# Optimization experiments

Hardware: AMD Instinct MI355X
Metric: run time of the kernel (lower is better)

## Reference

```python
import jax, jax.numpy as jnp
import numpy as np

N = 100_000      # nodes
E = 1_600_000    # edges
F_IN = 4         # num_features
H = 128          # hidden_channels
C = 5            # num_classes
G = 256          # graphs in batch


def setup_inputs() -> dict:
    key = jax.random.key(0)
    ks = jax.random.split(key, 14)
    x = jax.random.normal(ks[0], (N, F_IN), dtype=jnp.float32)
    edge_index = jax.random.randint(ks[1], (2, E), 0, N, dtype=jnp.int64)
    batch = jnp.sort(jax.random.randint(ks[2], (N,), 0, G, dtype=jnp.int64))
    def lin(k, fan_in, fan_out):
        kw, kb = jax.random.split(k)
        s = 1.0 / np.sqrt(fan_in)
        W = jax.random.uniform(kw, (fan_in, fan_out), jnp.float32, -s, s)
        b = jax.random.uniform(kb, (fan_out,), jnp.float32, -s, s)
        return W, b
    W1, b1 = lin(ks[3], F_IN, H)
    W2, b2 = lin(ks[4], H, H)
    W3, b3 = lin(ks[5], H, H)
    W4, b4 = lin(ks[6], H, H)
    Wl, bl = lin(ks[7], H, C)
    return {"x": x, "edge_index": edge_index, "batch": batch,
            "W1": W1, "b1": b1, "W2": W2, "b2": b2,
            "W3": W3, "b3": b3, "W4": W4, "b4": b4,
            "Wl": Wl, "bl": bl}


def reference(x, edge_index, batch, W1, b1, W2, b2, W3, b3, W4, b4, Wl, bl):
    n = x.shape[0]
    loop = jnp.arange(n, dtype=edge_index.dtype)
    src = jnp.concatenate([edge_index[0], loop])  # [E+N], with self-loops
    dst = jnp.concatenate([edge_index[1], loop])
    # symmetric normalization on A + I (PyG GCNConv default)
    deg = jax.ops.segment_sum(jnp.ones_like(dst, dtype=x.dtype), dst, num_segments=n)
    dinv = deg ** -0.5  # deg >= 1 thanks to self-loops
    coef = dinv[src] * dinv[dst]  # per-edge norm [E+N]

    def conv(h, W, b):
        h = h @ W                               # [N, H]
        msg = h[src] * coef[:, None]            # gather + scale [E+N, H]
        return jax.ops.segment_sum(msg, dst, num_segments=n) + b

    h = jax.nn.relu(conv(x, W1, b1))
    h = jax.nn.relu(conv(h, W2, b2))
    h = jax.nn.relu(conv(h, W3, b3))
    h = jax.nn.relu(conv(h, W4, b4))

    # global_mean_pool over graph ids
    counts = jax.ops.segment_sum(jnp.ones((n,), h.dtype), batch, num_segments=G)
    pooled = jax.ops.segment_sum(h, batch, num_segments=G)
    pooled = pooled / jnp.maximum(counts, 1.0)[:, None]  # [G, H]

    return jax.nn.sigmoid(pooled @ Wl + bl)  # [G, C]
```

## Files before the change

kernel.cpp:

```cpp
#include <hip/hip_runtime.h>
#include <hip/hip_fp8.h>
#include <math.h>

#define N_NODES 100000
#define N_EDGES 1600000
#define F_IN    4
#define HID     128
#define N_CLS   5
#define N_GRAPH 256
#define POOL_SEG 8

#define BSHIFT   9
#define BSIZE    512
#define NBUK     196
#define NCHUNK   200
#define CHUNK    8000

typedef _Float16 f16;
typedef _Float16 f16x2 __attribute__((ext_vector_type(2)));
typedef _Float16 f16x8 __attribute__((ext_vector_type(8)));
typedef float f32x4 __attribute__((ext_vector_type(4)));

__device__ __forceinline__ float rec_coef(unsigned r) {
    return (float)__builtin_bit_cast(_Float16, (unsigned short)(r & 0x7FFFu));
}

__device__ __forceinline__ f16x2 rec_coef2(unsigned r) {
    unsigned c = r & 0x7FFFu;
    return __builtin_bit_cast(f16x2, (c << 16) | c);
}

__device__ __forceinline__ float2 fp8x2_to_f32x2(unsigned short raw) {
    __hip_fp8x2_e4m3 t;
    t.__x = raw;
    return static_cast<float2>(t);
}

#if __has_builtin(__builtin_amdgcn_cvt_pk_f16_fp8)
__device__ __forceinline__ f16x2 cvt_h2(unsigned v) {
    auto t = __builtin_amdgcn_cvt_pk_f16_fp8((short)v);
    return __builtin_bit_cast(f16x2, t);
}
#else
__device__ __forceinline__ f16x2 cvt_h2(unsigned v) {
    float2 f = fp8x2_to_f32x2((unsigned short)v);
    auto t = __builtin_amdgcn_cvt_pkrtz(f.x, f.y);
    return __builtin_bit_cast(f16x2, t);
}
#endif

__device__ __forceinline__ void fma8h(f16x2 c2, uint2 v, f16x2* acc) {
    acc[0] += c2 * cvt_h2(v.x);
    acc[1] += c2 * cvt_h2(v.x >> 16);
    acc[2] += c2 * cvt_h2(v.y);
    acc[3] += c2 * cvt_h2(v.y >> 16);
}

__device__ __forceinline__ f16x2 shfl_xor_h2(f16x2 a, int m) {
    return __builtin_bit_cast(f16x2, __shfl_xor(__builtin_bit_cast(int, a), m, 64));
}

__global__ __launch_bounds__(256) void k_bc(const int* __restrict__ dst, int* __restrict__ C) {
    __shared__ int cnt[NBUK];
    int t = threadIdx.x;
    if (t < NBUK) cnt[t] = 0;
    __syncthreads();
    int base = blockIdx.x * CHUNK;
#pragma unroll
    for (int it = 0; it < 32; ++it) {
        int idx = it * 256 + t;
        if (idx < CHUNK) atomicAdd(&cnt[dst[base + idx] >> BSHIFT], 1);
    }
    __syncthreads();
    if (t < NBUK) C[blockIdx.x * NBUK + t] = cnt[t];
}

__global__ __launch_bounds__(256) void k_bscan(const int* __restrict__ C, int* __restrict__ Off,
                                               int* __restrict__ bbase) {
    __shared__ int s[256];
    int b = threadIdx.x;
    int tot = 0;
    if (b < NBUK) {
        for (int c = 0; c < NCHUNK; ++c) {
            Off[c * NBUK + b] = tot;
            tot += C[c * NBUK + b];
        }
    }
    s[b] = (b < NBUK) ? tot : 0;
    __syncthreads();
    for (int off = 1; off < 256; off <<= 1) {
        int v = (b >= off) ? s[b - off] : 0;
        __syncthreads();
        s[b] += v;
        __syncthreads();
    }
    if (b < NBUK) bbase[b] = s[b] - tot;
    if (b == 0) bbase[NBUK] = N_EDGES;
}

__global__ __launch_bounds__(256) void k_scatter(const int* __restrict__ src, const int* __restrict__ dst,
                                                 const int* __restrict__ Off, const int* __restrict__ bbase,
                                                 unsigned* __restrict__ bkt) {
    __shared__ int cur[NBUK];
    int t = threadIdx.x;
    if (t < NBUK) cur[t] = bbase[t] + Off[blockIdx.x * NBUK + t];
    __syncthreads();
    int base = blockIdx.x * CHUNK;
#pragma unroll
    for (int it = 0; it < 32; ++it) {
        int idx = it * 256 + t;
        if (idx < CHUNK) {
            int s = src[base + idx], d = dst[base + idx];
            int b = d >> BSHIFT;
            int p = atomicAdd(&cur[b], 1);
            bkt[p] = ((unsigned)s << BSHIFT) | (unsigned)(d & (BSIZE - 1));
        }
    }
}

__global__ __launch_bounds__(256) void k_hist2(const unsigned* __restrict__ bkt,
                                               const int* __restrict__ bbase,
                                               int* __restrict__ deg, float* __restrict__ dinv,
                                               int* __restrict__ padTot) {
    __shared__ int hist[BSIZE];
    __shared__ int tot;
    int t = threadIdx.x, b = blockIdx.x;
    hist[t] = 0; hist[t + 256] = 0;
    if (t == 0) tot = 0;
    __syncthreads();
    int s0 = bbase[b], s1 = bbase[b + 1];
    for (int e = s0 + t; e < s1; e += 256) atomicAdd(&hist[bkt[e] & (BSIZE - 1)], 1);
    __syncthreads();
    int loc = 0;
#pragma unroll
    for (int h = 0; h < 2; ++h) {
        int l = t + h * 256;
        int node = b * BSIZE + l;
        int d = hist[l];
        if (node < N_NODES) {
            deg[node] = d;
            dinv[node] = rsqrtf((float)d + 1.0f);
        }
        loc += (d + 7) >> 3;
    }
    atomicAdd(&tot, loc);
    __syncthreads();
    if (t == 0) padTot[b] = tot << 3;
}

__global__ __launch_bounds__(256) void k_pscan(const int* __restrict__ padTot, int* __restrict__ padBase,
                                               int* __restrict__ rowptrP) {
    __shared__ int s[256];
    int b = threadIdx.x;
    int v = (b < NBUK) ? padTot[b] : 0;
    s[b] = v;
    __syncthreads();
    for (int off = 1; off < 256; off <<= 1) {
        int u = (b >= off) ? s[b - off] : 0;
        __syncthreads();
        s[b] += u;
        __syncthreads();
    }
    if (b < NBUK) padBase[b] = s[b] - v;
    if (b == 0) {
        padBase[NBUK] = s[NBUK - 1];
        rowptrP[N_NODES] = s[NBUK - 1];
    }
}

__global__ __launch_bounds__(256) void k_local2(const unsigned* __restrict__ bkt,
                                                const int* __restrict__ bbase,
                                                const int* __restrict__ deg,
                                                const float* __restrict__ dinv,
                                                const int* __restrict__ padBase,
                                                int* __restrict__ rowptrP,
                                                unsigned* __restrict__ edges) {
    __shared__ int sc[BSIZE];
    __shared__ int cur[BSIZE];
    __shared__ int st[BSIZE];
    __shared__ float dv[BSIZE];
    int t = threadIdx.x, b = blockIdx.x;
    int base = padBase[b];
    int n0 = b * BSIZE + t, n1 = n0 + 256;
    int d0 = (n0 < N_NODES) ? deg[n0] : 0;
    int d1 = (n1 < N_NODES) ? deg[n1] : 0;
    int p0 = ((d0 + 7) >> 3) << 3;
    int p1 = ((d1 + 7) >> 3) << 3;
    sc[t] = p0; sc[t + 256] = p1;
    dv[t] = (n0 < N_NODES) ? dinv[n0] : 0.f;
    dv[t + 256] = (n1 < N_NODES) ? dinv[n1] : 0.f;
    __syncthreads();
    for (int off = 1; off < BSIZE; off <<= 1) {
        int i0 = t, i1 = t + 256;
        int v0 = (i0 >= off) ? sc[i0 - off] : 0;
        int v1 = (i1 >= off) ? sc[i1 - off] : 0;
        __syncthreads();
        sc[i0] += v0; sc[i1] += v1;
        __syncthreads();
    }
    int off0 = base + sc[t] - p0;
    int off1 = base + sc[t + 256] - p1;
    if (n0 < N_NODES) rowptrP[n0] = off0;
    if (n1 < N_NODES) rowptrP[n1] = off1;
    cur[t] = off0; cur[t + 256] = off1;
    st[t]  = off0; st[t + 256]  = off1;
    int padT = sc[BSIZE - 1];
    for (int i = base + t; i < base + padT; i += 256) edges[i] = 0;
    __syncthreads();
    int s0 = bbase[b], s1 = bbase[b + 1];
    for (int e = s0 + t; e < s1; e += 256) {
        unsigned r = bkt[e];
        int dl = (int)(r & (BSIZE - 1));
        int s = (int)(r >> BSHIFT);
        int p = atomicAdd(&cur[dl], 1);
        int rs = st[dl];
        int sl = p - rs;
        int phys = rs + (sl & ~7) + (((sl & 1) << 2) | ((sl >> 1) & 3));
        float c = dv[dl] * dinv[s];
        unsigned short cb = __builtin_bit_cast(unsigned short, (f16)c);
        edges[phys] = ((unsigned)s << 15) | (unsigned)(cb & 0x7FFFu);
    }
}

__global__ __launch_bounds__(256) void k_aggx1(const float4* __restrict__ x,
                                               const int* __restrict__ rowptrP,
                                               const unsigned* __restrict__ edges,
                                               const float* __restrict__ dinv,
                                               const float* __restrict__ W1, const float* __restrict__ b1,
                                               unsigned* __restrict__ hA) {
    __shared__ float4 sxa[16];
    __shared__ float sW[4 * HID];
    __shared__ float sb[HID];
    int t = threadIdx.x;
    sW[t] = W1[t];
    sW[t + 256] = W1[t + 256];
    if (t < HID) sb[t] = b1[t];
    int grp = t >> 4;
    int l = t & 15;
    int node = blockIdx.x * 16 + grp;
    int beg = rowptrP[node], end = rowptrP[node + 1];
    float ax = 0.f, ay = 0.f, az = 0.f, aw = 0.f;
    for (int e = beg + l; e < end; e += 16) {
        unsigned r = edges[e];
        float c = rec_coef(r);
        float4 v = x[r >> 15];
        ax = fmaf(c, v.x, ax); ay = fmaf(c, v.y, ay);
        az = fmaf(c, v.z, az); aw = fmaf(c, v.w, aw);
    }
#pragma unroll
    for (int off = 1; off < 16; off <<= 1) {
        ax += __shfl_xor(ax, off, 64);
        ay += __shfl_xor(ay, off, 64);
        az += __shfl_xor(az, off, 64);
        aw += __shfl_xor(aw, off, 64);
    }
    if (l == 0) {
        float di = dinv[node];
        float c0 = di * di;
        float4 xv = x[node];
        sxa[grp] = make_float4(fmaf(c0, xv.x, ax), fmaf(c0, xv.y, ay),
                               fmaf(c0, xv.z, az), fmaf(c0, xv.w, aw));
    }
    __syncthreads();

    int node0 = blockIdx.x * 16;
#pragma unroll
    for (int it = 0; it < 2; ++it) {
        int id = it * 256 + t;
        int n = id >> 5;
        int g = id & 31;
        float4 a = sxa[n];
        float c[4];
#pragma unroll
        for (int j = 0; j < 4; ++j) {
            int col = g * 4 + j;
            float v = sb[col];
            v = fmaf(a.x, sW[col],           v);
            v = fmaf(a.y, sW[HID + col],     v);
            v = fmaf(a.z, sW[2 * HID + col], v);
            v = fmaf(a.w, sW[3 * HID + col], v);
            c[j] = fmaxf(v, 0.0f);
        }
        unsigned lo = __hip_fp8x2_e4m3(make_float2(c[0], c[1])).__x;
        unsigned hi = __hip_fp8x2_e4m3(make_float2(c[2], c[3])).__x;
        hA[(node0 + n) * 32 + g] = lo | (hi << 16);
    }
}

template <bool FP8OUT>
__global__ __launch_bounds__(512, 8) void k_aggemm8(const unsigned* __restrict__ h8,
                                                    const int* __restrict__ rowptrP,
                                                    const unsigned* __restrict__ edges,
                                                    const float* __restrict__ dinv,
                                                    const f16* __restrict__ Wp,
                                                    const float* __restrict__ bias,
                                                    void* __restrict__ outv) {
    __shared__ f16 S[16 * HID];
    int wave = threadIdx.x >> 6;
    int lane = threadIdx.x & 63;
    int half = lane >> 5;
    int g    = (lane >> 4) & 1;
    int l    = lane & 15;
    int node0 = blockIdx.x * 16;
    int row   = wave * 2 + half;
    int node  = node0 + row;
    int beg = rowptrP[node];
    int end = rowptrP[node + 1];
    const char* hp = (const char*)h8 + l * 8;

    f16x2 acc[4];
    acc[0] = (f16x2){0, 0}; acc[1] = (f16x2){0, 0};
    acc[2] = (f16x2){0, 0}; acc[3] = (f16x2){0, 0};
    {
        float di = dinv[node];
        f16 c0 = (g == 0) ? (f16)(di * di) : (f16)0.f;
        f16x2 c02; c02.x = c0; c02.y = c0;
        uint2 v = *(const uint2*)(hp + ((size_t)node << 7));
        fma8h(c02, v, acc);
    }

    if (beg < end) {
        uint4 R = *(const uint4*)(edges + beg + g * 4);
        uint2 V0 = *(const uint2*)(hp + ((R.x >> 8) & 0xFFFFFF80u));
        uint2 V1 = *(const uint2*)(hp + ((R.y >> 8) & 0xFFFFFF80u));
        uint2 V2 = *(const uint2*)(hp + ((R.z >> 8) & 0xFFFFFF80u));
        uint2 V3 = *(const uint2*)(hp + ((R.w >> 8) & 0xFFFFFF80u));
        int e = beg;
        while (true) {
            int en = e + 8;
            bool more = en < end;
            uint4 Rc = R;
            uint2 W0 = V0, W1 = V1, W2 = V2, W3 = V3;
            if (more) R = *(const uint4*)(edges + en + g * 4);
            fma8h(rec_coef2(Rc.x), W0, acc);
            fma8h(rec_coef2(Rc.y), W1, acc);
            fma8h(rec_coef2(Rc.z), W2, acc);
            fma8h(rec_coef2(Rc.w), W3, acc);
            if (!more) break;
            V0 = *(const uint2*)(hp + ((R.x >> 8) & 0xFFFFFF80u));
            V1 = *(const uint2*)(hp + ((R.y >> 8) & 0xFFFFFF80u));
            V2 = *(const uint2*)(hp + ((R.z >> 8) & 0xFFFFFF80u));
            V3 = *(const uint2*)(hp + ((R.w >> 8) & 0xFFFFFF80u));
            e = en;
        }
    }

#pragma unroll
    for (int j = 0; j < 4; ++j) acc[j] += shfl_xor_h2(acc[j], 16);

    if ((lane & 16) == 0) {
        f16x8 o;
        o[0] = acc[0][0]; o[1] = acc[0][1]; o[2] = acc[1][0]; o[3] = acc[1][1];
        o[4] = acc[2][0]; o[5] = acc[2][1]; o[6] = acc[3][0]; o[7] = acc[3][1];
        int dw = (l * 4) ^ ((row & 7) << 2);
        *(f16x8*)&S[row * HID + dw * 2] = o;
    }
    __syncthreads();

    {
        int t = wave;
        int m = lane & 15;
        int q = lane >> 4;
        f32x4 c4 = (f32x4){0.f, 0.f, 0.f, 0.f};
#pragma unroll
        for (int ks = 0; ks < 4; ++ks) {
            int dw = (ks * 16 + q * 4) ^ ((m & 7) << 2);
            f16x8 a = *(const f16x8*)&S[m * HID + dw * 2];
            f16x8 b = *(const f16x8*)(Wp + ((size_t)(t * 4 + ks) * 64 + lane) * 8);
            c4 = __builtin_amdgcn_mfma_f32_16x16x32_f16(a, b, c4, 0, 0, 0);
        }
        float bb = bias[t * 16 + m];
#pragma unroll
        for (int r = 0; r < 4; ++r) {
            float val = fmaxf(c4[r] + bb, 0.0f);
            int orow = node0 + q * 4 + r;
            if constexpr (FP8OUT) {
                ((__hip_fp8_e4m3*)outv)[(size_t)orow * HID + t * 16 + m] = __hip_fp8_e4m3(val);
            } else {
                ((f16*)outv)[(size_t)orow * HID + t * 16 + m] = (f16)val;
            }
        }
    }
}

__global__ __launch_bounds__(256) void k_packW3(const float* __restrict__ W2, const float* __restrict__ W3,
                                                const float* __restrict__ W4, f16* __restrict__ Wp) {
    int idx = blockIdx.x * 256 + threadIdx.x;
    int which = idx >> 14;
    int r = idx & 16383;
    const float* W = (which == 0) ? W2 : (which == 1) ? W3 : W4;
    int j  = r & 7;
    int L  = (r >> 3) & 63;
    int ks = (r >> 9) & 3;
    int ct = r >> 11;
    int k = ks * 32 + (L >> 4) * 8 + j;
    int n = ct * 16 + (L & 15);
    Wp[idx] = (f16)W[k * HID + n];
}

__device__ __forceinline__ int lower_bound_batch(const int* __restrict__ batch, int val) {
    int lo = 0, hi = N_NODES;
    while (lo < hi) { int m = (lo + hi) >> 1; if (batch[m] < val) lo = m + 1; else hi = m; }
    return lo;
}

__global__ __launch_bounds__(128) void k_pool1(const f16* __restrict__ h, const int* __restrict__ batch,
                                               float* __restrict__ partials) {
    int g = blockIdx.x / POOL_SEG;
    int s = blockIdx.x % POOL_SEG;
    int f = threadIdx.x;
    int beg = lower_bound_batch(batch, g);
    int end = lower_bound_batch(batch, g + 1);
    int len = end - beg;
    int sb = beg + (int)(((long long)len * s) / POOL_SEG);
    int se = beg + (int)(((long long)len * (s + 1)) / POOL_SEG);
    float acc = 0.0f;
    for (int i = sb; i < se; ++i) acc += (float)h[i * HID + f];
    partials[(size_t)blockIdx.x * HID + f] = acc;
}

__global__ __launch_bounds__(128) void k_pool2h(const float* __restrict__ partials,
                                                const int* __restrict__ batch,
                                                const float* __restrict__ Wl, const float* __restrict__ bl,
                                                float* __restrict__ out) {
    __shared__ float sp[HID];
    int g = blockIdx.x;
    int f = threadIdx.x;
    float acc = 0.0f;
#pragma unroll
    for (int s = 0; s < POOL_SEG; ++s)
        acc += partials[(size_t)(g * POOL_SEG + s) * HID + f];
    int beg = lower_bound_batch(batch, g);
    int end = lower_bound_batch(batch, g + 1);
    sp[f] = acc / fmaxf((float)(end - beg), 1.0f);
    __syncthreads();
    if (f < N_CLS) {
        float v = bl[f];
        for (int k = 0; k < HID; ++k) v = fmaf(sp[k], Wl[k * N_CLS + f], v);
        out[g * N_CLS + f] = 1.0f / (1.0f + expf(-v));
    }
}

extern "C" void kernel_launch(void* const* d_in, const int* in_sizes, int n_in,
                              void* d_out, int out_size, void* d_ws, size_t ws_size,
                              hipStream_t stream) {
    const float* x     = (const float*)d_in[0];
    const int*   ei    = (const int*)d_in[1];
    const int*   batch = (const int*)d_in[2];
    const float* W1 = (const float*)d_in[3];  const float* b1 = (const float*)d_in[4];
    const float* W2 = (const float*)d_in[5];  const float* b2 = (const float*)d_in[6];
    const float* W3 = (const float*)d_in[7];  const float* b3 = (const float*)d_in[8];
    const float* W4 = (const float*)d_in[9];  const float* b4 = (const float*)d_in[10];
    const float* Wl = (const float*)d_in[11]; const float* bl = (const float*)d_in[12];
    float* out = (float*)d_out;

    const size_t EPAD = (size_t)N_EDGES + (size_t)N_NODES * 16;

    char* p = (char*)d_ws;
    auto alloc = [&](size_t bytes) { char* r = p; p += (bytes + 255) & ~(size_t)255; return (void*)r; };
    int*      C       = (int*)     alloc((size_t)NCHUNK * NBUK * 4);
    int*      Off     = (int*)     alloc((size_t)NCHUNK * NBUK * 4);
    int*      bbase   = (int*)     alloc((size_t)(NBUK + 1) * 4);
    int*      padTot  = (int*)     alloc((size_t)NBUK * 4);
    int*      padBase = (int*)     alloc((size_t)(NBUK + 1) * 4);
    unsigned* bkt     = (unsigned*)alloc((size_t)N_EDGES * 4);
    int*      deg     = (int*)     alloc((size_t)N_NODES * 4);
    int*      rowptrP = (int*)     alloc((size_t)(N_NODES + 1) * 4);
    float*    dinv    = (float*)   alloc((size_t)N_NODES * 4);
    unsigned* edges   = (unsigned*)alloc(EPAD * 4);
    unsigned* hA      = (unsigned*)alloc((size_t)N_NODES * HID);
    unsigned* hC      = (unsigned*)alloc((size_t)N_NODES * HID);
    f16*      h4      = (f16*)     alloc((size_t)N_NODES * HID * 2);
    float*    parts   = (float*)   alloc((size_t)N_GRAPH * POOL_SEG * HID * 4);
    f16*      Wp      = (f16*)     alloc((size_t)3 * HID * HID * 2);
    f16*      Wp2 = Wp;
    f16*      Wp3 = Wp + HID * HID;
    f16*      Wp4 = Wp + 2 * HID * HID;

    const int* srcv = ei;
    const int* dstv = ei + N_EDGES;

    k_bc     <<<NCHUNK, 256, 0, stream>>>(dstv, C);
    k_bscan  <<<1, 256, 0, stream>>>(C, Off, bbase);
    k_scatter<<<NCHUNK, 256, 0, stream>>>(srcv, dstv, Off, bbase, bkt);
    k_hist2  <<<NBUK, 256, 0, stream>>>(bkt, bbase, deg, dinv, padTot);
    k_pscan  <<<1, 256, 0, stream>>>(padTot, padBase, rowptrP);
    k_local2 <<<NBUK, 256, 0, stream>>>(bkt, bbase, deg, dinv, padBase, rowptrP, edges);

    k_packW3<<<192, 256, 0, stream>>>(W2, W3, W4, Wp);

    k_aggx1<<<N_NODES / 16, 256, 0, stream>>>((const float4*)x, rowptrP, edges, dinv, W1, b1, hA);

    const int fgrid = N_NODES / 16;
    k_aggemm8<true ><<<fgrid, 512, 0, stream>>>(hA, rowptrP, edges, dinv, Wp2, b2, hC);
    k_aggemm8<true ><<<fgrid, 512, 0, stream>>>(hC, rowptrP, edges, dinv, Wp3, b3, hA);
    k_aggemm8<false><<<fgrid, 512, 0, stream>>>(hA, rowptrP, edges, dinv, Wp4, b4, h4);

    k_pool1 <<<N_GRAPH * POOL_SEG, 128, 0, stream>>>(h4, batch, parts);
    k_pool2h<<<N_GRAPH, 128, 0, stream>>>(parts, batch, Wl, bl, out);
}
```

Baseline: 319.3 us.

## Replace bucketed two-pass CSR build with global-atomic degree count and direct fill

The CSR construction no longer scatters edges into 512-node buckets and then locally sorts them. It now counts degrees with global atomics, runs a three-stage scan to get padded row pointers, and fills the padded edge array directly using per-node global atomic cursors. This drops the intermediate bucket array and one full pass over the edges. In exchange it uses random global atomics and scattered writes, which can contend and lose locality compared with bucket-local shared-memory atomics.

```diff
diff --git a/kernel.cpp b/kernel.cpp
--- a/kernel.cpp
+++ b/kernel.cpp
@@ -13,8 +13,7 @@
 #define BSHIFT   9
 #define BSIZE    512
 #define NBUK     196
-#define NCHUNK   200
-#define CHUNK    8000
+#define EPAD8   (N_EDGES + 7 * N_NODES)
 
 typedef _Float16 f16;
 typedef _Float16 f16x2 __attribute__((ext_vector_type(2)));
@@ -60,135 +59,34 @@
     return __builtin_bit_cast(f16x2, __shfl_xor(__builtin_bit_cast(int, a), m, 64));
 }
 
-__global__ __launch_bounds__(256) void k_bc(const int* __restrict__ dst, int* __restrict__ C) {
-    __shared__ int cnt[NBUK];
-    int t = threadIdx.x;
-    if (t < NBUK) cnt[t] = 0;
-    __syncthreads();
-    int base = blockIdx.x * CHUNK;
-#pragma unroll
-    for (int it = 0; it < 32; ++it) {
-        int idx = it * 256 + t;
-        if (idx < CHUNK) atomicAdd(&cnt[dst[base + idx] >> BSHIFT], 1);
-    }
-    __syncthreads();
-    if (t < NBUK) C[blockIdx.x * NBUK + t] = cnt[t];
-}
-
-__global__ __launch_bounds__(256) void k_bscan(const int* __restrict__ C, int* __restrict__ Off,
-                                               int* __restrict__ bbase) {
-    __shared__ int s[256];
-    int b = threadIdx.x;
-    int tot = 0;
-    if (b < NBUK) {
-        for (int c = 0; c < NCHUNK; ++c) {
-            Off[c * NBUK + b] = tot;
-            tot += C[c * NBUK + b];
-        }
-    }
-    s[b] = (b < NBUK) ? tot : 0;
-    __syncthreads();
-    for (int off = 1; off < 256; off <<= 1) {
-        int v = (b >= off) ? s[b - off] : 0;
-        __syncthreads();
-        s[b] += v;
-        __syncthreads();
-    }
-    if (b < NBUK) bbase[b] = s[b] - tot;
-    if (b == 0) bbase[NBUK] = N_EDGES;
-}
-
-__global__ __launch_bounds__(256) void k_scatter(const int* __restrict__ src, const int* __restrict__ dst,
-                                                 const int* __restrict__ Off, const int* __restrict__ bbase,
-                                                 unsigned* __restrict__ bkt) {
-    __shared__ int cur[NBUK];
-    int t = threadIdx.x;
-    if (t < NBUK) cur[t] = bbase[t] + Off[blockIdx.x * NBUK + t];
-    __syncthreads();
-    int base = blockIdx.x * CHUNK;
-#pragma unroll
-    for (int it = 0; it < 32; ++it) {
-        int idx = it * 256 + t;
-        if (idx < CHUNK) {
-            int s = src[base + idx], d = dst[base + idx];
-            int b = d >> BSHIFT;
-            int p = atomicAdd(&cur[b], 1);
-            bkt[p] = ((unsigned)s << BSHIFT) | (unsigned)(d & (BSIZE - 1));
-        }
-    }
-}
-
-__global__ __launch_bounds__(256) void k_hist2(const unsigned* __restrict__ bkt,
-                                               const int* __restrict__ bbase,
-                                               int* __restrict__ deg, float* __restrict__ dinv,
-                                               int* __restrict__ padTot) {
-    __shared__ int hist[BSIZE];
-    __shared__ int tot;
+__global__ __launch_bounds__(256) void k_init(int* __restrict__ deg, uint4* __restrict__ edges4) {
+    int i = blockIdx.x * 256 + threadIdx.x;
+    int stride = gridDim.x * 256;
+    for (int j = i; j < N_NODES; j += stride) deg[j] = 0;
+    const int n4 = (EPAD8 + 3) / 4;
+    uint4 z = {0u, 0u, 0u, 0u};
+    for (int j = i; j < n4; j += stride) edges4[j] = z;
+}
+
+__global__ __launch_bounds__(256) void k_deg(const int* __restrict__ dst, int* __restrict__ deg) {
+    int i = blockIdx.x * 256 + threadIdx.x;
+    atomicAdd(&deg[dst[i]], 1);
+}
+
+__global__ __launch_bounds__(256) void k_scan1(const int* __restrict__ deg,
+                                               int* __restrict__ rowptrP,
+                                               float* __restrict__ dinv,
+                                               int* __restrict__ bsum) {
+    __shared__ int sc[BSIZE];
     int t = threadIdx.x, b = blockIdx.x;
-    hist[t] = 0; hist[t + 256] = 0;
-    if (t == 0) tot = 0;
-    __syncthreads();
-    int s0 = bbase[b], s1 = bbase[b + 1];
-    for (int e = s0 + t; e < s1; e += 256) atomicAdd(&hist[bkt[e] & (BSIZE - 1)], 1);
-    __syncthreads();
-    int loc = 0;
-#pragma unroll
-    for (int h = 0; h < 2; ++h) {
-        int l = t + h * 256;
-        int node = b * BSIZE + l;
-        int d = hist[l];
-        if (node < N_NODES) {
-            deg[node] = d;
-            dinv[node] = rsqrtf((float)d + 1.0f);
-        }
-        loc += (d + 7) >> 3;
-    }
-    atomicAdd(&tot, loc);
-    __syncthreads();
-    if (t == 0) padTot[b] = tot << 3;
-}
-
-__global__ __launch_bounds__(256) void k_pscan(const int* __restrict__ padTot, int* __restrict__ padBase,
-                                               int* __restrict__ rowptrP) {
-    __shared__ int s[256];
-    int b = threadIdx.x;
-    int v = (b < NBUK) ? padTot[b] : 0;
-    s[b] = v;
-    __syncthreads();
-    for (int off = 1; off < 256; off <<= 1) {
-        int u = (b >= off) ? s[b - off] : 0;
-        __syncthreads();
-        s[b] += u;
-        __syncthreads();
-    }
-    if (b < NBUK) padBase[b] = s[b] - v;
-    if (b == 0) {
-        padBase[NBUK] = s[NBUK - 1];
-        rowptrP[N_NODES] = s[NBUK - 1];
-    }
-}
-
-__global__ __launch_bounds__(256) void k_local2(const unsigned* __restrict__ bkt,
-                                                const int* __restrict__ bbase,
-                                                const int* __restrict__ deg,
-                                                const float* __restrict__ dinv,
-                                                const int* __restrict__ padBase,
-                                                int* __restrict__ rowptrP,
-                                                unsigned* __restrict__ edges) {
-    __shared__ int sc[BSIZE];
-    __shared__ int cur[BSIZE];
-    __shared__ int st[BSIZE];
-    __shared__ float dv[BSIZE];
-    int t = threadIdx.x, b = blockIdx.x;
-    int base = padBase[b];
     int n0 = b * BSIZE + t, n1 = n0 + 256;
     int d0 = (n0 < N_NODES) ? deg[n0] : 0;
     int d1 = (n1 < N_NODES) ? deg[n1] : 0;
     int p0 = ((d0 + 7) >> 3) << 3;
     int p1 = ((d1 + 7) >> 3) << 3;
     sc[t] = p0; sc[t + 256] = p1;
-    dv[t] = (n0 < N_NODES) ? dinv[n0] : 0.f;
-    dv[t + 256] = (n1 < N_NODES) ? dinv[n1] : 0.f;
+    if (n0 < N_NODES) dinv[n0] = rsqrtf((float)d0 + 1.0f);
+    if (n1 < N_NODES) dinv[n1] = rsqrtf((float)d1 + 1.0f);
     __syncthreads();
     for (int off = 1; off < BSIZE; off <<= 1) {
         int i0 = t, i1 = t + 256;
@@ -198,28 +96,53 @@
         sc[i0] += v0; sc[i1] += v1;
         __syncthreads();
     }
-    int off0 = base + sc[t] - p0;
-    int off1 = base + sc[t + 256] - p1;
-    if (n0 < N_NODES) rowptrP[n0] = off0;
-    if (n1 < N_NODES) rowptrP[n1] = off1;
-    cur[t] = off0; cur[t + 256] = off1;
-    st[t]  = off0; st[t + 256]  = off1;
-    int padT = sc[BSIZE - 1];
-    for (int i = base + t; i < base + padT; i += 256) edges[i] = 0;
+    if (n0 < N_NODES) rowptrP[n0] = sc[t] - p0;
+    if (n1 < N_NODES) rowptrP[n1] = sc[t + 256] - p1;
+    if (t == 0) bsum[b] = sc[BSIZE - 1];
+}
+
+__global__ __launch_bounds__(256) void k_scan2(const int* __restrict__ bsum, int* __restrict__ padBase) {
+    __shared__ int s[256];
+    int b = threadIdx.x;
+    int v = (b < NBUK) ? bsum[b] : 0;
+    s[b] = v;
     __syncthreads();
-    int s0 = bbase[b], s1 = bbase[b + 1];
-    for (int e = s0 + t; e < s1; e += 256) {
-        unsigned r = bkt[e];
-        int dl = (int)(r & (BSIZE - 1));
-        int s = (int)(r >> BSHIFT);
-        int p = atomicAdd(&cur[dl], 1);
-        int rs = st[dl];
-        int sl = p - rs;
-        int phys = rs + (sl & ~7) + (((sl & 1) << 2) | ((sl >> 1) & 3));
-        float c = dv[dl] * dinv[s];
-        unsigned short cb = __builtin_bit_cast(unsigned short, (f16)c);
-        edges[phys] = ((unsigned)s << 15) | (unsigned)(cb & 0x7FFFu);
-    }
+    for (int off = 1; off < 256; off <<= 1) {
+        int u = (b >= off) ? s[b - off] : 0;
+        __syncthreads();
+        s[b] += u;
+        __syncthreads();
+    }
+    if (b < NBUK) padBase[b] = s[b] - v;
+    if (b == 0) padBase[NBUK] = s[NBUK - 1];
+}
+
+__global__ __launch_bounds__(256) void k_scan3(int* __restrict__ rowptrP,
+                                               const int* __restrict__ padBase,
+                                               int* __restrict__ cur) {
+    int node = blockIdx.x * 256 + threadIdx.x;
+    if (node < N_NODES) {
+        int v = rowptrP[node] + padBase[node >> BSHIFT];
+        rowptrP[node] = v;
+        cur[node] = v;
+    }
+    if (node == 0) rowptrP[N_NODES] = padBase[NBUK];
+}
+
+__global__ __launch_bounds__(256) void k_fill(const int* __restrict__ src, const int* __restrict__ dst,
+                                              const float* __restrict__ dinv,
+                                              const int* __restrict__ rowptrP,
+                                              int* __restrict__ cur,
+                                              unsigned* __restrict__ edges) {
+    int i = blockIdx.x * 256 + threadIdx.x;
+    int s = src[i], d = dst[i];
+    float c = dinv[d] * dinv[s];
+    int p = atomicAdd(&cur[d], 1);
+    int rs = rowptrP[d];
+    int sl = p - rs;
+    int phys = rs + (sl & ~7) + (((sl & 1) << 2) | ((sl >> 1) & 3));
+    unsigned short cb = __builtin_bit_cast(unsigned short, (f16)c);
+    edges[phys] = ((unsigned)s << 15) | (unsigned)(cb & 0x7FFFu);
 }
 
 __global__ __launch_bounds__(256) void k_aggx1(const float4* __restrict__ x,
@@ -454,20 +377,17 @@
     const float* Wl = (const float*)d_in[11]; const float* bl = (const float*)d_in[12];
     float* out = (float*)d_out;
 
-    const size_t EPAD = (size_t)N_EDGES + (size_t)N_NODES * 16;
+    const size_t ECAP = (size_t)EPAD8 + 256;
 
     char* p = (char*)d_ws;
     auto alloc = [&](size_t bytes) { char* r = p; p += (bytes + 255) & ~(size_t)255; return (void*)r; };
-    int*      C       = (int*)     alloc((size_t)NCHUNK * NBUK * 4);
-    int*      Off     = (int*)     alloc((size_t)NCHUNK * NBUK * 4);
-    int*      bbase   = (int*)     alloc((size_t)(NBUK + 1) * 4);
-    int*      padTot  = (int*)     alloc((size_t)NBUK * 4);
-    int*      padBase = (int*)     alloc((size_t)(NBUK + 1) * 4);
-    unsigned* bkt     = (unsigned*)alloc((size_t)N_EDGES * 4);
     int*      deg     = (int*)     alloc((size_t)N_NODES * 4);
     int*      rowptrP = (int*)     alloc((size_t)(N_NODES + 1) * 4);
+    int*      cur     = (int*)     alloc((size_t)N_NODES * 4);
     float*    dinv    = (float*)   alloc((size_t)N_NODES * 4);
-    unsigned* edges   = (unsigned*)alloc(EPAD * 4);
+    int*      bsum    = (int*)     alloc((size_t)NBUK * 4);
+    int*      padBase = (int*)     alloc((size_t)(NBUK + 1) * 4);
+    unsigned* edges   = (unsigned*)alloc(ECAP * 4);
     unsigned* hA      = (unsigned*)alloc((size_t)N_NODES * HID);
     unsigned* hC      = (unsigned*)alloc((size_t)N_NODES * HID);
     f16*      h4      = (f16*)     alloc((size_t)N_NODES * HID * 2);
@@ -480,12 +400,12 @@
     const int* srcv = ei;
     const int* dstv = ei + N_EDGES;
 
-    k_bc     <<<NCHUNK, 256, 0, stream>>>(dstv, C);
-    k_bscan  <<<1, 256, 0, stream>>>(C, Off, bbase);
-    k_scatter<<<NCHUNK, 256, 0, stream>>>(srcv, dstv, Off, bbase, bkt);
-    k_hist2  <<<NBUK, 256, 0, stream>>>(bkt, bbase, deg, dinv, padTot);
-    k_pscan  <<<1, 256, 0, stream>>>(padTot, padBase, rowptrP);
-    k_local2 <<<NBUK, 256, 0, stream>>>(bkt, bbase, deg, dinv, padBase, rowptrP, edges);
+    k_init <<<2048, 256, 0, stream>>>(deg, (uint4*)edges);
+    k_deg  <<<N_EDGES / 256, 256, 0, stream>>>(dstv, deg);
+    k_scan1<<<NBUK, 256, 0, stream>>>(deg, rowptrP, dinv, bsum);
+    k_scan2<<<1, 256, 0, stream>>>(bsum, padBase);
+    k_scan3<<<392, 256, 0, stream>>>(rowptrP, padBase, cur);
+    k_fill <<<N_EDGES / 256, 256, 0, stream>>>(srcv, dstv, dinv, rowptrP, cur, edges);
 
     k_packW3<<<192, 256, 0, stream>>>(W2, W3, W4, Wp);
 
```

Measured after the change: 410.9 us. 28.7% more time.

## Compute degrees during bucket count and parallelize chunk-offset scan across buckets

Applied to the files above, without the earlier changes.

Per-node degrees are now counted with global atomics in the first bucket-count pass, so the separate histogram pass over the bucketed edges is no longer needed. The serial single-block scan over 200 chunks per bucket is replaced by a multi-block kernel that scans each bucket's chunk counts in parallel and also computes dinv and padded totals. One combined scan kernel then produces both bucket bases and padded bases. The trade is 1.6M global atomics on deg plus an extra memset, in exchange for removing one kernel and a serial loop.

```diff
diff --git a/kernel.cpp b/kernel.cpp
--- a/kernel.cpp
+++ b/kernel.cpp
@@ -60,7 +60,9 @@
     return __builtin_bit_cast(f16x2, __shfl_xor(__builtin_bit_cast(int, a), m, 64));
 }
 
-__global__ __launch_bounds__(256) void k_bc(const int* __restrict__ dst, int* __restrict__ C) {
+
+__global__ __launch_bounds__(256) void k_bc2(const int* __restrict__ dst, int* __restrict__ CT,
+                                             int* __restrict__ deg) {
     __shared__ int cnt[NBUK];
     int t = threadIdx.x;
     if (t < NBUK) cnt[t] = 0;
@@ -69,33 +71,81 @@
 #pragma unroll
     for (int it = 0; it < 32; ++it) {
         int idx = it * 256 + t;
-        if (idx < CHUNK) atomicAdd(&cnt[dst[base + idx] >> BSHIFT], 1);
-    }
-    __syncthreads();
-    if (t < NBUK) C[blockIdx.x * NBUK + t] = cnt[t];
-}
-
-__global__ __launch_bounds__(256) void k_bscan(const int* __restrict__ C, int* __restrict__ Off,
-                                               int* __restrict__ bbase) {
+        if (idx < CHUNK) {
+            int d = dst[base + idx];
+            atomicAdd(&cnt[d >> BSHIFT], 1);
+            atomicAdd(&deg[d], 1);
+        }
+    }
+    __syncthreads();
+    if (t < NBUK) CT[t * NCHUNK + blockIdx.x] = cnt[t];
+}
+
+__global__ __launch_bounds__(256) void k_mid(const int* __restrict__ CT, const int* __restrict__ deg,
+                                             int* __restrict__ Off, int* __restrict__ bucketTot,
+                                             float* __restrict__ dinv, int* __restrict__ padTot) {
     __shared__ int s[256];
-    int b = threadIdx.x;
-    int tot = 0;
-    if (b < NBUK) {
-        for (int c = 0; c < NCHUNK; ++c) {
-            Off[c * NBUK + b] = tot;
-            tot += C[c * NBUK + b];
-        }
-    }
-    s[b] = (b < NBUK) ? tot : 0;
+    __shared__ int pt;
+    int t = threadIdx.x, b = blockIdx.x;
+    if (t == 0) pt = 0;
+    int v = (t < NCHUNK) ? CT[b * NCHUNK + t] : 0;
+    s[t] = v;
     __syncthreads();
     for (int off = 1; off < 256; off <<= 1) {
-        int v = (b >= off) ? s[b - off] : 0;
-        __syncthreads();
-        s[b] += v;
-        __syncthreads();
-    }
-    if (b < NBUK) bbase[b] = s[b] - tot;
-    if (b == 0) bbase[NBUK] = N_EDGES;
+        int u = (t >= off) ? s[t - off] : 0;
+        __syncthreads();
+        s[t] += u;
+        __syncthreads();
+    }
+    if (t < NCHUNK) Off[t * NBUK + b] = s[t] - v;
+    if (t == 255) bucketTot[b] = s[255];
+    int loc = 0;
+#pragma unroll
+    for (int h = 0; h < 2; ++h) {
+        int node = b * BSIZE + t + h * 256;
+        if (node < N_NODES) {
+            int d = deg[node];
+            dinv[node] = rsqrtf((float)d + 1.0f);
+            loc += (d + 7) >> 3;
+        }
+    }
+    atomicAdd(&pt, loc);
+    __syncthreads();
+    if (t == 0) padTot[b] = pt << 3;
+}
+
+__global__ __launch_bounds__(256) void k_scan2x(const int* __restrict__ bucketTot,
+                                                const int* __restrict__ padTot,
+                                                int* __restrict__ bbase, int* __restrict__ padBase,
+                                                int* __restrict__ rowptrP) {
+    __shared__ int s[256];
+    int t = threadIdx.x;
+    int v = (t < NBUK) ? bucketTot[t] : 0;
+    s[t] = v;
+    __syncthreads();
+    for (int off = 1; off < 256; off <<= 1) {
+        int u = (t >= off) ? s[t - off] : 0;
+        __syncthreads();
+        s[t] += u;
+        __syncthreads();
+    }
+    if (t < NBUK) bbase[t] = s[t] - v;
+    if (t == 0) bbase[NBUK] = N_EDGES;
+    __syncthreads();
+    int w = (t < NBUK) ? padTot[t] : 0;
+    s[t] = w;
+    __syncthreads();
+    for (int off = 1; off < 256; off <<= 1) {
+        int u = (t >= off) ? s[t - off] : 0;
+        __syncthreads();
+        s[t] += u;
+        __syncthreads();
+    }
+    if (t < NBUK) padBase[t] = s[t] - w;
+    if (t == 0) {
+        padBase[NBUK] = s[NBUK - 1];
+        rowptrP[N_NODES] = s[NBUK - 1];
+    }
 }
 
 __global__ __launch_bounds__(256) void k_scatter(const int* __restrict__ src, const int* __restrict__ dst,
@@ -115,56 +165,6 @@
             int p = atomicAdd(&cur[b], 1);
             bkt[p] = ((unsigned)s << BSHIFT) | (unsigned)(d & (BSIZE - 1));
         }
-    }
-}
-
-__global__ __launch_bounds__(256) void k_hist2(const unsigned* __restrict__ bkt,
-                                               const int* __restrict__ bbase,
-                                               int* __restrict__ deg, float* __restrict__ dinv,
-                                               int* __restrict__ padTot) {
-    __shared__ int hist[BSIZE];
-    __shared__ int tot;
-    int t = threadIdx.x, b = blockIdx.x;
-    hist[t] = 0; hist[t + 256] = 0;
-    if (t == 0) tot = 0;
-    __syncthreads();
-    int s0 = bbase[b], s1 = bbase[b + 1];
-    for (int e = s0 + t; e < s1; e += 256) atomicAdd(&hist[bkt[e] & (BSIZE - 1)], 1);
-    __syncthreads();
-    int loc = 0;
-#pragma unroll
-    for (int h = 0; h < 2; ++h) {
-        int l = t + h * 256;
-        int node = b * BSIZE + l;
-        int d = hist[l];
-        if (node < N_NODES) {
-            deg[node] = d;
-            dinv[node] = rsqrtf((float)d + 1.0f);
-        }
-        loc += (d + 7) >> 3;
-    }
-    atomicAdd(&tot, loc);
-    __syncthreads();
-    if (t == 0) padTot[b] = tot << 3;
-}
-
-__global__ __launch_bounds__(256) void k_pscan(const int* __restrict__ padTot, int* __restrict__ padBase,
-                                               int* __restrict__ rowptrP) {
-    __shared__ int s[256];
-    int b = threadIdx.x;
-    int v = (b < NBUK) ? padTot[b] : 0;
-    s[b] = v;
-    __syncthreads();
-    for (int off = 1; off < 256; off <<= 1) {
-        int u = (b >= off) ? s[b - off] : 0;
-        __syncthreads();
-        s[b] += u;
-        __syncthreads();
-    }
-    if (b < NBUK) padBase[b] = s[b] - v;
-    if (b == 0) {
-        padBase[NBUK] = s[NBUK - 1];
-        rowptrP[N_NODES] = s[NBUK - 1];
     }
 }
 
@@ -458,9 +458,10 @@
 
     char* p = (char*)d_ws;
     auto alloc = [&](size_t bytes) { char* r = p; p += (bytes + 255) & ~(size_t)255; return (void*)r; };
-    int*      C       = (int*)     alloc((size_t)NCHUNK * NBUK * 4);
+    int*      CT      = (int*)     alloc((size_t)NCHUNK * NBUK * 4);
     int*      Off     = (int*)     alloc((size_t)NCHUNK * NBUK * 4);
     int*      bbase   = (int*)     alloc((size_t)(NBUK + 1) * 4);
+    int*      bucketTot = (int*)   alloc((size_t)NBUK * 4);
     int*      padTot  = (int*)     alloc((size_t)NBUK * 4);
     int*      padBase = (int*)     alloc((size_t)(NBUK + 1) * 4);
     unsigned* bkt     = (unsigned*)alloc((size_t)N_EDGES * 4);
@@ -480,12 +481,12 @@
     const int* srcv = ei;
     const int* dstv = ei + N_EDGES;
 
-    k_bc     <<<NCHUNK, 256, 0, stream>>>(dstv, C);
-    k_bscan  <<<1, 256, 0, stream>>>(C, Off, bbase);
+    hipMemsetAsync(deg, 0, (size_t)N_NODES * 4, stream);
+    k_bc2   <<<NCHUNK, 256, 0, stream>>>(dstv, CT, deg);
+    k_mid   <<<NBUK, 256, 0, stream>>>(CT, deg, Off, bucketTot, dinv, padTot);
+    k_scan2x<<<1, 256, 0, stream>>>(bucketTot, padTot, bbase, padBase, rowptrP);
     k_scatter<<<NCHUNK, 256, 0, stream>>>(srcv, dstv, Off, bbase, bkt);
-    k_hist2  <<<NBUK, 256, 0, stream>>>(bkt, bbase, deg, dinv, padTot);
-    k_pscan  <<<1, 256, 0, stream>>>(padTot, padBase, rowptrP);
-    k_local2 <<<NBUK, 256, 0, stream>>>(bkt, bbase, deg, dinv, padBase, rowptrP, edges);
+    k_local2<<<NBUK, 256, 0, stream>>>(bkt, bbase, deg, dinv, padBase, rowptrP, edges);
 
     k_packW3<<<192, 256, 0, stream>>>(W2, W3, W4, Wp);
 
```

After: 364.9 us. 1.14x slower.

## Fuse bucket count, scan and scatter into one pass with fixed-capacity buckets

Applied to the files above, without the earlier changes.

Replaces the three-kernel count/scan/scatter bucketing with a single kernel. Each block counts locally, then reserves space in each bucket with one global atomicAdd into fixed-capacity slots of BUKCAP entries. This removes two kernel launches, the serial single-block scan and a second read of dst. The bucket cursors are initialised inside the weight-packing kernel. In exchange it assumes no bucket receives more than BUKCAP edges, so a skewed edge distribution would overflow into the next bucket.

```diff
diff --git a/kernel.cpp b/kernel.cpp
--- a/kernel.cpp
+++ b/kernel.cpp
@@ -15,6 +15,7 @@
 #define NBUK     196
 #define NCHUNK   200
 #define CHUNK    8000
+#define BUKCAP   9216
 
 typedef _Float16 f16;
 typedef _Float16 f16x2 __attribute__((ext_vector_type(2)));
@@ -60,8 +61,11 @@
     return __builtin_bit_cast(f16x2, __shfl_xor(__builtin_bit_cast(int, a), m, 64));
 }
 
-__global__ __launch_bounds__(256) void k_bc(const int* __restrict__ dst, int* __restrict__ C) {
+
+__global__ __launch_bounds__(256) void k_scatterA(const int* __restrict__ src, const int* __restrict__ dst,
+                                                  int* __restrict__ gcur, unsigned* __restrict__ bkt) {
     __shared__ int cnt[NBUK];
+    __shared__ int cur[NBUK];
     int t = threadIdx.x;
     if (t < NBUK) cnt[t] = 0;
     __syncthreads();
@@ -72,40 +76,8 @@
         if (idx < CHUNK) atomicAdd(&cnt[dst[base + idx] >> BSHIFT], 1);
     }
     __syncthreads();
-    if (t < NBUK) C[blockIdx.x * NBUK + t] = cnt[t];
-}
-
-__global__ __launch_bounds__(256) void k_bscan(const int* __restrict__ C, int* __restrict__ Off,
-                                               int* __restrict__ bbase) {
-    __shared__ int s[256];
-    int b = threadIdx.x;
-    int tot = 0;
-    if (b < NBUK) {
-        for (int c = 0; c < NCHUNK; ++c) {
-            Off[c * NBUK + b] = tot;
-            tot += C[c * NBUK + b];
-        }
-    }
-    s[b] = (b < NBUK) ? tot : 0;
-    __syncthreads();
-    for (int off = 1; off < 256; off <<= 1) {
-        int v = (b >= off) ? s[b - off] : 0;
-        __syncthreads();
-        s[b] += v;
-        __syncthreads();
-    }
-    if (b < NBUK) bbase[b] = s[b] - tot;
-    if (b == 0) bbase[NBUK] = N_EDGES;
-}
-
-__global__ __launch_bounds__(256) void k_scatter(const int* __restrict__ src, const int* __restrict__ dst,
-                                                 const int* __restrict__ Off, const int* __restrict__ bbase,
-                                                 unsigned* __restrict__ bkt) {
-    __shared__ int cur[NBUK];
-    int t = threadIdx.x;
-    if (t < NBUK) cur[t] = bbase[t] + Off[blockIdx.x * NBUK + t];
-    __syncthreads();
-    int base = blockIdx.x * CHUNK;
+    if (t < NBUK) cur[t] = atomicAdd(&gcur[t], cnt[t]);
+    __syncthreads();
 #pragma unroll
     for (int it = 0; it < 32; ++it) {
         int idx = it * 256 + t;
@@ -119,7 +91,7 @@
 }
 
 __global__ __launch_bounds__(256) void k_hist2(const unsigned* __restrict__ bkt,
-                                               const int* __restrict__ bbase,
+                                               const int* __restrict__ gcur,
                                                int* __restrict__ deg, float* __restrict__ dinv,
                                                int* __restrict__ padTot) {
     __shared__ int hist[BSIZE];
@@ -128,7 +100,7 @@
     hist[t] = 0; hist[t + 256] = 0;
     if (t == 0) tot = 0;
     __syncthreads();
-    int s0 = bbase[b], s1 = bbase[b + 1];
+    int s0 = b * BUKCAP, s1 = gcur[b];
     for (int e = s0 + t; e < s1; e += 256) atomicAdd(&hist[bkt[e] & (BSIZE - 1)], 1);
     __syncthreads();
     int loc = 0;
@@ -169,7 +141,7 @@
 }
 
 __global__ __launch_bounds__(256) void k_local2(const unsigned* __restrict__ bkt,
-                                                const int* __restrict__ bbase,
+                                                const int* __restrict__ gcur,
                                                 const int* __restrict__ deg,
                                                 const float* __restrict__ dinv,
                                                 const int* __restrict__ padBase,
@@ -207,7 +179,7 @@
     int padT = sc[BSIZE - 1];
     for (int i = base + t; i < base + padT; i += 256) edges[i] = 0;
     __syncthreads();
-    int s0 = bbase[b], s1 = bbase[b + 1];
+    int s0 = b * BUKCAP, s1 = gcur[b];
     for (int e = s0 + t; e < s1; e += 256) {
         unsigned r = bkt[e];
         int dl = (int)(r & (BSIZE - 1));
@@ -384,7 +356,9 @@
 }
 
 __global__ __launch_bounds__(256) void k_packW3(const float* __restrict__ W2, const float* __restrict__ W3,
-                                                const float* __restrict__ W4, f16* __restrict__ Wp) {
+                                                const float* __restrict__ W4, f16* __restrict__ Wp,
+                                                int* __restrict__ gcur) {
+    if (blockIdx.x == 0 && threadIdx.x < NBUK) gcur[threadIdx.x] = threadIdx.x * BUKCAP;
     int idx = blockIdx.x * 256 + threadIdx.x;
     int which = idx >> 14;
     int r = idx & 16383;
@@ -458,12 +432,10 @@
 
     char* p = (char*)d_ws;
     auto alloc = [&](size_t bytes) { char* r = p; p += (bytes + 255) & ~(size_t)255; return (void*)r; };
-    int*      C       = (int*)     alloc((size_t)NCHUNK * NBUK * 4);
-    int*      Off     = (int*)     alloc((size_t)NCHUNK * NBUK * 4);
-    int*      bbase   = (int*)     alloc((size_t)(NBUK + 1) * 4);
+    int*      gcur    = (int*)     alloc((size_t)NBUK * 4);
     int*      padTot  = (int*)     alloc((size_t)NBUK * 4);
     int*      padBase = (int*)     alloc((size_t)(NBUK + 1) * 4);
-    unsigned* bkt     = (unsigned*)alloc((size_t)N_EDGES * 4);
+    unsigned* bkt     = (unsigned*)alloc((size_t)NBUK * BUKCAP * 4);
     int*      deg     = (int*)     alloc((size_t)N_NODES * 4);
     int*      rowptrP = (int*)     alloc((size_t)(N_NODES + 1) * 4);
     float*    dinv    = (float*)   alloc((size_t)N_NODES * 4);
@@ -480,14 +452,11 @@
     const int* srcv = ei;
     const int* dstv = ei + N_EDGES;
 
-    k_bc     <<<NCHUNK, 256, 0, stream>>>(dstv, C);
-    k_bscan  <<<1, 256, 0, stream>>>(C, Off, bbase);
-    k_scatter<<<NCHUNK, 256, 0, stream>>>(srcv, dstv, Off, bbase, bkt);
-    k_hist2  <<<NBUK, 256, 0, stream>>>(bkt, bbase, deg, dinv, padTot);
-    k_pscan  <<<1, 256, 0, stream>>>(padTot, padBase, rowptrP);
-    k_local2 <<<NBUK, 256, 0, stream>>>(bkt, bbase, deg, dinv, padBase, rowptrP, edges);
-
-    k_packW3<<<192, 256, 0, stream>>>(W2, W3, W4, Wp);
+    k_packW3  <<<192, 256, 0, stream>>>(W2, W3, W4, Wp, gcur);
+    k_scatterA<<<NCHUNK, 256, 0, stream>>>(srcv, dstv, gcur, bkt);
+    k_hist2   <<<NBUK, 256, 0, stream>>>(bkt, gcur, deg, dinv, padTot);
+    k_pscan   <<<1, 256, 0, stream>>>(padTot, padBase, rowptrP);
+    k_local2  <<<NBUK, 256, 0, stream>>>(bkt, gcur, deg, dinv, padBase, rowptrP, edges);
 
     k_aggx1<<<N_NODES / 16, 256, 0, stream>>>((const float4*)x, rowptrP, edges, dinv, W1, b1, hA);
 
```

Measured after the change: 307.5 us. 3.7% less time.
